# Kernel tuning notes

Measured on AMD Instinct MI355X. Metric: run time of the kernel, lower is better.

## Reference

```python
import jax, jax.numpy as jnp
import numpy as np

# Model constants (match init_kwargs)
DIM = 256
H = 8
HD = DIM // H          # 32
WIN = 5                # spatial window_size
QS = 4                 # quant_size
CQS = 2 * QS           # color_quant_size = 8
CWIN = 2               # color_windowsize
W = 64                 # voxels per window (equal-size windows for the reference)
L_XYZ = WIN * QS       # 20 -> table length 40
L_RGB = CWIN * CQS     # 16 -> table length 32


def setup_inputs() -> dict:
    key = jax.random.key(0)
    ks = jax.random.split(key, 12)
    N = 8192
    feats = jax.random.normal(ks[0], (N, DIM), dtype=jnp.float32)
    xyz = jax.random.uniform(ks[1], (N, 3), dtype=jnp.float32) * WIN    # [0, window_size)
    rgb = jax.random.uniform(ks[2], (N, 3), dtype=jnp.float32) * CWIN   # [0, color_windowsize)
    n_coords = jnp.concatenate([xyz, rgb], axis=1)
    std = 0.02
    xyz_shape = (3, 2 * L_XYZ, H, HD)
    rgb_shape = (3, 2 * L_RGB, H, HD)
    return {
        "feats": feats,
        "n_coords": n_coords,
        "qkv_w": jax.random.normal(ks[3], (3 * DIM, DIM), dtype=jnp.float32) * std,
        "qkv_b": jnp.zeros((3 * DIM,), dtype=jnp.float32),
        "q_xyz_t": jax.random.normal(ks[4], xyz_shape, dtype=jnp.float32) * std,
        "k_xyz_t": jax.random.normal(ks[5], xyz_shape, dtype=jnp.float32) * std,
        "v_xyz_t": jax.random.normal(ks[6], xyz_shape, dtype=jnp.float32) * std,
        "q_rgb_t": jax.random.normal(ks[7], rgb_shape, dtype=jnp.float32) * std,
        "k_rgb_t": jax.random.normal(ks[8], rgb_shape, dtype=jnp.float32) * std,
        "v_rgb_t": jax.random.normal(ks[9], rgb_shape, dtype=jnp.float32) * std,
        "proj_w": jax.random.normal(ks[10], (DIM, DIM), dtype=jnp.float32) * std,
        "proj_b": jnp.zeros((DIM,), dtype=jnp.float32),
    }


def _attn_bias(q, k, idx, q_table, k_table):
    """Relative-signal bias added to QK logits.
    q,k: [nw, W, H, hd]; idx: [nw, W, W, 3] int; tables: [3, T, H, hd].
    bias[n,h,i,j] = sum_c q[n,i,h]. q_table[c, idx[n,i,j,c], h] + k[n,j,h]. k_table[c, idx, h]
    Returns (bias [nw,H,W,W], one_hot [nw,W,W,3,T]) so the one-hot is reused for the value bias.
    """
    T = q_table.shape[1]
    oh = jax.nn.one_hot(idx, T, dtype=q.dtype)                # [nw,W,W,3,T]
    dq = jnp.einsum('nihd,cthd->nicht', q, q_table)           # per-voxel dot vs all table rows
    dk = jnp.einsum('njhd,cthd->njcht', k, k_table)
    bias_q = jnp.einsum('nicht,nijct->nhij', dq, oh)
    bias_k = jnp.einsum('njcht,nijct->nhij', dk, oh)
    return bias_q + bias_k, oh


def _value_bias(attn, oh, v_table):
    """out[n,i,h,:] += sum_j attn[n,h,i,j] * sum_c v_table[c, idx[n,i,j,c], h, :]"""
    at = jnp.einsum('nhij,nijct->nhict', attn, oh)            # scatter attn mass onto table rows
    return jnp.einsum('nhict,cthd->nihd', at, v_table)


def reference(feats, n_coords, qkv_w, qkv_b, q_xyz_t, k_xyz_t, v_xyz_t,
              q_rgb_t, k_rgb_t, v_rgb_t, proj_w, proj_b):
    N = feats.shape[0]
    nw = N // W
    scale = HD ** (-0.5)

    # QKV projection, split into per-window heads
    qkv = (feats @ qkv_w.T + qkv_b).reshape(nw, W, 3, H, HD)
    q = qkv[:, :, 0] * scale
    k = qkv[:, :, 1]
    v = qkv[:, :, 2]

    # Quantized relative-signal indices (coordinate deltas, offset to [0, 2L))
    scaled = jnp.concatenate(
        [n_coords[:, 0:3] * QS, n_coords[:, 3:6] * CQS], axis=1)   # [N, 6]
    cw = scaled.reshape(nw, W, 6)
    delta = jnp.floor(cw[:, :, None, :] - cw[:, None, :, :]).astype(jnp.int32)
    offs = jnp.array([L_XYZ] * 3 + [L_RGB] * 3, dtype=jnp.int32)
    hi = jnp.array([2 * L_XYZ - 1] * 3 + [2 * L_RGB - 1] * 3, dtype=jnp.int32)
    idx = jnp.clip(delta + offs, 0, hi)                        # [nw, W, W, 6]
    idx_xyz, idx_rgb = idx[..., :3], idx[..., 3:]

    bias_x, oh_x = _attn_bias(q, k, idx_xyz, q_xyz_t, k_xyz_t)
    bias_r, oh_r = _attn_bias(q, k, idx_rgb, q_rgb_t, k_rgb_t)

    logits = jnp.einsum('nihd,njhd->nhij', q, k) + bias_x + bias_r
    attn = jax.nn.softmax(logits, axis=-1)

    out = (jnp.einsum('nhij,njhd->nihd', attn, v)
           + _value_bias(attn, oh_x, v_xyz_t)
           + _value_bias(attn, oh_r, v_rgb_t))
    out = out.reshape(N, DIM)
    return out @ proj_w.T + proj_b
```

## Files before the change

### kernel.cpp

```cpp
#include <hip/hip_runtime.h>


typedef __attribute__((ext_vector_type(8))) short short8;
typedef __attribute__((ext_vector_type(4))) float f32x4;

__device__ __forceinline__ unsigned short f2bf(float f) {
    union { float f; unsigned int u; } v; v.f = f;
    unsigned int r = v.u + 0x7FFFu + ((v.u >> 16) & 1u);
    return (unsigned short)(r >> 16);
}

#define LFENCE() asm volatile("s_waitcnt lgkmcnt(0)" ::: "memory")

__global__ __launch_bounds__(256) void k_qkv(
    const float* __restrict__ A, const float* __restrict__ B,
    const float* __restrict__ bias,
    ushort* __restrict__ qb, ushort* __restrict__ kb, ushort* __restrict__ vb)
{
    __shared__ __align__(16) ushort a_s[128 * 72];
    __shared__ __align__(16) ushort b_s[64 * 72];
    const int tid = threadIdx.x;
    const int m0 = blockIdx.y * 128;
    const int n0 = blockIdx.x * 64;
    const int w = tid >> 6, wm = w >> 1, wn = w & 1;
    const int l4 = tid & 15, quad = (tid >> 4) & 3;
    f32x4 acc[4][2];
#pragma unroll
    for (int mt = 0; mt < 4; ++mt)
#pragma unroll
        for (int nt = 0; nt < 2; ++nt) acc[mt][nt] = (f32x4){0.f, 0.f, 0.f, 0.f};

    for (int k0 = 0; k0 < 256; k0 += 64) {
#pragma unroll
        for (int l = 0; l < 4; ++l) {
            int e = tid + l * 256;
            int row = e >> 3, kq = e & 7;
            const float* ap = A + (size_t)(m0 + row) * 256 + k0 + kq * 8;
            float4 v0 = *(const float4*)ap, v1 = *(const float4*)(ap + 4);
            union { ushort u[8]; uint4 v; } pk;
            pk.u[0] = f2bf(v0.x); pk.u[1] = f2bf(v0.y); pk.u[2] = f2bf(v0.z); pk.u[3] = f2bf(v0.w);
            pk.u[4] = f2bf(v1.x); pk.u[5] = f2bf(v1.y); pk.u[6] = f2bf(v1.z); pk.u[7] = f2bf(v1.w);
            *(uint4*)&a_s[row * 72 + kq * 8] = pk.v;
        }
#pragma unroll
        for (int l = 0; l < 2; ++l) {
            int e = tid + l * 256;
            int row = e >> 3, kq = e & 7;
            const float* bp = B + (size_t)(n0 + row) * 256 + k0 + kq * 8;
            float4 v0 = *(const float4*)bp, v1 = *(const float4*)(bp + 4);
            union { ushort u[8]; uint4 v; } pk;
            pk.u[0] = f2bf(v0.x); pk.u[1] = f2bf(v0.y); pk.u[2] = f2bf(v0.z); pk.u[3] = f2bf(v0.w);
            pk.u[4] = f2bf(v1.x); pk.u[5] = f2bf(v1.y); pk.u[6] = f2bf(v1.z); pk.u[7] = f2bf(v1.w);
            *(uint4*)&b_s[row * 72 + kq * 8] = pk.v;
        }
        __syncthreads();
#pragma unroll
        for (int kh = 0; kh < 2; ++kh) {
            short8 bf0 = *(const short8*)&b_s[(wn * 32 + l4) * 72 + kh * 32 + quad * 8];
            short8 bf1 = *(const short8*)&b_s[(wn * 32 + 16 + l4) * 72 + kh * 32 + quad * 8];
#pragma unroll
            for (int mt = 0; mt < 4; ++mt) {
                short8 af = *(const short8*)&a_s[(wm * 64 + mt * 16 + l4) * 72 + kh * 32 + quad * 8];
                acc[mt][0] = __builtin_amdgcn_mfma_f32_16x16x32_bf16(af, bf0, acc[mt][0], 0, 0, 0);
                acc[mt][1] = __builtin_amdgcn_mfma_f32_16x16x32_bf16(af, bf1, acc[mt][1], 0, 0, 0);
            }
        }
        __syncthreads();
    }
#pragma unroll
    for (int nt = 0; nt < 2; ++nt) {
        int c = n0 + wn * 32 + nt * 16 + l4;
        float bv = bias[c];
        int s = c >> 8, rem = c & 255, h = rem >> 5, d = rem & 31;
        ushort* dst = (s == 0) ? qb : ((s == 1) ? kb : vb);
        float mul = (s == 0) ? 0.17677669529663687f : 1.0f;
#pragma unroll
        for (int mt = 0; mt < 4; ++mt) {
            int mbase = m0 + wm * 64 + mt * 16 + quad * 4;
#pragma unroll
            for (int reg = 0; reg < 4; ++reg) {
                int m = mbase + reg;
                int nw = m >> 6, ii = m & 63;
                dst[((size_t)((nw * 8 + h) * 64 + ii)) * 32 + d] = f2bf((acc[mt][nt][reg] + bv) * mul);
            }
        }
    }
}

#define DBS 44
#define FXS 16777216.0f
#define FXI (1.0f / 16777216.0f)

__global__ __launch_bounds__(256, 2) void k_bias(
    const ushort* __restrict__ qb, const ushort* __restrict__ kb,
    const float* __restrict__ nco,
    const float* __restrict__ kxt, const float* __restrict__ krt,
    float* __restrict__ lgt)
{
    __shared__ __align__(16) float dbuf[64 * DBS];
    __shared__ __align__(16) ushort q_s[64 * 40];
    __shared__ __align__(16) ushort k_s[64 * 40];
    __shared__ __align__(16) ushort tbl[128 * 40];
    __shared__ __align__(16) float cwf[64 * 6];

    const int tid = threadIdx.x;
    const int n = blockIdx.x >> 3;
    const int h = blockIdx.x & 7;
    const int w = tid >> 6;
    const int l4 = tid & 15;
    const int quad = (tid >> 4) & 3;

    const size_t base = (size_t)((n * 8 + h) * 64) * 32;

    {
        int row = tid >> 2, part = tid & 3;
        *(uint4*)&q_s[row * 40 + part * 8] = *(const uint4*)(qb + base + tid * 8);
        *(uint4*)&k_s[row * 40 + part * 8] = *(const uint4*)(kb + base + tid * 8);
    }
    if (tid < 64) {
        const float* cp = nco + (size_t)(n * 64 + tid) * 6;
        cwf[tid * 6 + 0] = cp[0] * 4.f; cwf[tid * 6 + 1] = cp[1] * 4.f;
        cwf[tid * 6 + 2] = cp[2] * 4.f; cwf[tid * 6 + 3] = cp[3] * 8.f;
        cwf[tid * 6 + 4] = cp[4] * 8.f; cwf[tid * 6 + 5] = cp[5] * 8.f;
    }

    auto stageTbl = [&](const float* tbg, int R, int Rpad) {
        for (int e = tid; e < R * 4; e += 256) {
            int r = e >> 2, part = e & 3;
            const float* src = tbg + (size_t)r * 256 + part * 8;
            float4 f0 = *(const float4*)src, f1 = *(const float4*)(src + 4);
            union { ushort u[8]; uint4 v; } pk;
            pk.u[0] = f2bf(f0.x); pk.u[1] = f2bf(f0.y); pk.u[2] = f2bf(f0.z); pk.u[3] = f2bf(f0.w);
            pk.u[4] = f2bf(f1.x); pk.u[5] = f2bf(f1.y); pk.u[6] = f2bf(f1.z); pk.u[7] = f2bf(f1.w);
            *(uint4*)&tbl[r * 40 + part * 8] = pk.v;
        }
        for (int e = tid; e < (Rpad - R) * 40; e += 256) tbl[R * 40 + e] = 0;
    };

    float lg[4][4];
    int ibase[4];
#pragma unroll
    for (int r = 0; r < 4; ++r) ibase[r] = (w * 16 + quad * 4 + r) * DBS;

    auto tgemmC = [&](const ushort* a_s, int c, int T) {
        short8 af = *(const short8*)&a_s[(w * 16 + l4) * 40 + quad * 8];
        const int NT = (T == 40) ? 3 : 2;
        for (int tt = 0; tt < NT; ++tt) {
            short8 bf = *(const short8*)&tbl[(c * T + tt * 16 + l4) * 40 + quad * 8];
            f32x4 a = {0.f, 0.f, 0.f, 0.f};
            a = __builtin_amdgcn_mfma_f32_16x16x32_bf16(af, bf, a, 0, 0, 0);
            int col = tt * 16 + l4;
            int rb = w * 16 + quad * 4;
            if (col < T) {
                dbuf[(rb + 0) * DBS + col] = a[0];
                dbuf[(rb + 1) * DBS + col] = a[1];
                dbuf[(rb + 2) * DBS + col] = a[2];
                dbuf[(rb + 3) * DBS + col] = a[3];
            }
        }
    };

    stageTbl(kxt + h * 32, 120, 128);
    __syncthreads();

    unsigned idxp[24];
    {
        float co[4][6], cl[4][6];
#pragma unroll
        for (int r = 0; r < 4; ++r) {
            int j = w * 16 + quad * 4 + r;
#pragma unroll
            for (int c6 = 0; c6 < 6; ++c6) co[r][c6] = cwf[j * 6 + c6];
        }
#pragma unroll
        for (int tt = 0; tt < 4; ++tt) {
            int i = tt * 16 + l4;
#pragma unroll
            for (int c6 = 0; c6 < 6; ++c6) cl[tt][c6] = cwf[i * 6 + c6];
        }
#pragma unroll
        for (int c6 = 0; c6 < 6; ++c6) {
            const int off = (c6 < 3) ? 20 : 16, hi = (c6 < 3) ? 39 : 31;
#pragma unroll
            for (int tt = 0; tt < 4; ++tt) {
                unsigned p = 0;
#pragma unroll
                for (int r = 0; r < 4; ++r) {
                    int x = min(max((int)floorf(cl[tt][c6] - co[r][c6]) + off, 0), hi);
                    p |= (unsigned)x << (8 * r);
                }
                idxp[c6 * 4 + tt] = p;
            }
        }
    }

    auto gatherT = [&](int cc) {
#pragma unroll
        for (int tt = 0; tt < 4; ++tt) {
            unsigned p = idxp[cc * 4 + tt];
#pragma unroll
            for (int r = 0; r < 4; ++r) {
                int x = (p >> (8 * r)) & 255;
                lg[tt][r] += dbuf[ibase[r] + x];
            }
        }
    };

    {
        short8 ak = *(const short8*)&k_s[(w * 16 + l4) * 40 + quad * 8];
#pragma unroll
        for (int tt = 0; tt < 4; ++tt) {
            short8 bq = *(const short8*)&q_s[(tt * 16 + l4) * 40 + quad * 8];
            f32x4 r = {0.f, 0.f, 0.f, 0.f};
            r = __builtin_amdgcn_mfma_f32_16x16x32_bf16(ak, bq, r, 0, 0, 0);
            lg[tt][0] = r[0]; lg[tt][1] = r[1]; lg[tt][2] = r[2]; lg[tt][3] = r[3];
        }
    }

    tgemmC(k_s, 0, 40); LFENCE();
    gatherT(0); LFENCE();
    tgemmC(k_s, 1, 40); LFENCE();
    gatherT(1); LFENCE();
    tgemmC(k_s, 2, 40); LFENCE();
    gatherT(2);
    __syncthreads();
    stageTbl(krt + h * 32, 96, 96);
    __syncthreads();
    tgemmC(k_s, 0, 32); LFENCE();
    gatherT(3); LFENCE();
    tgemmC(k_s, 1, 32); LFENCE();
    gatherT(4); LFENCE();
    tgemmC(k_s, 2, 32); LFENCE();
    gatherT(5);

    {
        float* lp = lgt + (size_t)(n * 8 + h) * 4096;
#pragma unroll
        for (int tt = 0; tt < 4; ++tt)
#pragma unroll
            for (int reg = 0; reg < 4; ++reg)
                lp[(w * 16 + quad * 4 + reg) * 64 + tt * 16 + l4] = lg[tt][reg];
    }
}

__global__ __launch_bounds__(256, 2) void k_av(
    const ushort* __restrict__ qb, const ushort* __restrict__ vb,
    const float* __restrict__ nco,
    const float* __restrict__ qxt, const float* __restrict__ vxt,
    const float* __restrict__ qrt, const float* __restrict__ vrt,
    const float* __restrict__ lgt,
    ushort* __restrict__ aout)
{
    __shared__ __align__(16) float dbuf[64 * DBS];
    __shared__ __align__(16) ushort U[11264];
    __shared__ __align__(16) float cwf[64 * 6];
    ushort* q_s  = U;
    ushort* tbl  = U + 2560;
    ushort* attn_s = U;
    ushort* v_t    = U + 4608;
    ushort* vtbl   = U + 6912;

    const int tid = threadIdx.x;
    const int n = blockIdx.x >> 3;
    const int h = blockIdx.x & 7;
    const int w = tid >> 6;
    const int lane = tid & 63;
    const int l4 = tid & 15;
    const int quad = (tid >> 4) & 3;

    const size_t base = (size_t)((n * 8 + h) * 64) * 32;

    {
        int row = tid >> 2, part = tid & 3;
        *(uint4*)&q_s[row * 40 + part * 8] = *(const uint4*)(qb + base + tid * 8);
    }
    if (tid < 64) {
        const float* cp = nco + (size_t)(n * 64 + tid) * 6;
        cwf[tid * 6 + 0] = cp[0] * 4.f; cwf[tid * 6 + 1] = cp[1] * 4.f;
        cwf[tid * 6 + 2] = cp[2] * 4.f; cwf[tid * 6 + 3] = cp[3] * 8.f;
        cwf[tid * 6 + 4] = cp[4] * 8.f; cwf[tid * 6 + 5] = cp[5] * 8.f;
    }

    auto stageTbl = [&](const float* tbg, int R, int Rpad) {
        for (int e = tid; e < R * 4; e += 256) {
            int r = e >> 2, part = e & 3;
            const float* src = tbg + (size_t)r * 256 + part * 8;
            float4 f0 = *(const float4*)src, f1 = *(const float4*)(src + 4);
            union { ushort u[8]; uint4 v; } pk;
            pk.u[0] = f2bf(f0.x); pk.u[1] = f2bf(f0.y); pk.u[2] = f2bf(f0.z); pk.u[3] = f2bf(f0.w);
            pk.u[4] = f2bf(f1.x); pk.u[5] = f2bf(f1.y); pk.u[6] = f2bf(f1.z); pk.u[7] = f2bf(f1.w);
            *(uint4*)&tbl[r * 40 + part * 8] = pk.v;
        }
        for (int e = tid; e < (Rpad - R) * 40; e += 256) tbl[R * 40 + e] = 0;
    };
    auto stageVtbl = [&](const float* tbg, int R) {
        for (int e = tid; e < R * 4; e += 256) {
            int r = e >> 2, part = e & 3;
            const float* src = tbg + (size_t)r * 256 + part * 8;
            float4 f0 = *(const float4*)src, f1 = *(const float4*)(src + 4);
            int d0 = part * 8;
            vtbl[(d0 + 0) * 136 + r] = f2bf(f0.x);
            vtbl[(d0 + 1) * 136 + r] = f2bf(f0.y);
            vtbl[(d0 + 2) * 136 + r] = f2bf(f0.z);
            vtbl[(d0 + 3) * 136 + r] = f2bf(f0.w);
            vtbl[(d0 + 4) * 136 + r] = f2bf(f1.x);
            vtbl[(d0 + 5) * 136 + r] = f2bf(f1.y);
            vtbl[(d0 + 6) * 136 + r] = f2bf(f1.z);
            vtbl[(d0 + 7) * 136 + r] = f2bf(f1.w);
        }
    };
    auto stageVt = [&]() {
        int j = tid >> 2, d0 = (tid & 3) * 8;
        uint4 pk = *(const uint4*)(vb + base + tid * 8);
        const ushort* u = (const ushort*)&pk;
#pragma unroll
        for (int ii = 0; ii < 8; ++ii) v_t[(d0 + ii) * 72 + j] = u[ii];
    };

    float lg[4][4];
    {
        const float* lp = lgt + (size_t)(n * 8 + h) * 4096;
        int i0 = w * 16 + quad * 4;
#pragma unroll
        for (int tt = 0; tt < 4; ++tt) {
            f32x4 v = *(const f32x4*)(lp + (size_t)(tt * 16 + l4) * 64 + i0);
            lg[tt][0] = v[0]; lg[tt][1] = v[1]; lg[tt][2] = v[2]; lg[tt][3] = v[3];
        }
    }

    int ibase[4];
#pragma unroll
    for (int r = 0; r < 4; ++r) ibase[r] = (w * 16 + quad * 4 + r) * DBS;

    auto tgemmC = [&](const ushort* a_s, int c, int T) {
        short8 af = *(const short8*)&a_s[(w * 16 + l4) * 40 + quad * 8];
        const int NT = (T == 40) ? 3 : 2;
        for (int tt = 0; tt < NT; ++tt) {
            short8 bf = *(const short8*)&tbl[(c * T + tt * 16 + l4) * 40 + quad * 8];
            f32x4 a = {0.f, 0.f, 0.f, 0.f};
            a = __builtin_amdgcn_mfma_f32_16x16x32_bf16(af, bf, a, 0, 0, 0);
            int col = tt * 16 + l4;
            int rb = w * 16 + quad * 4;
            if (col < T) {
                dbuf[(rb + 0) * DBS + col] = a[0];
                dbuf[(rb + 1) * DBS + col] = a[1];
                dbuf[(rb + 2) * DBS + col] = a[2];
                dbuf[(rb + 3) * DBS + col] = a[3];
            }
        }
    };
    auto zeroOwn = [&]() {
        float4 z = {0.f, 0.f, 0.f, 0.f};
        float4* rb = (float4*)&dbuf[w * 16 * DBS];
        for (int v = lane; v < 176; v += 64) rb[v] = z;
    };

    stageTbl(qxt + h * 32, 120, 128);
    __syncthreads();

    unsigned idxp[24];
    {
        float co[4][6], cl[4][6];
#pragma unroll
        for (int r = 0; r < 4; ++r) {
            int i = w * 16 + quad * 4 + r;
#pragma unroll
            for (int c6 = 0; c6 < 6; ++c6) co[r][c6] = cwf[i * 6 + c6];
        }
#pragma unroll
        for (int tt = 0; tt < 4; ++tt) {
            int j = tt * 16 + l4;
#pragma unroll
            for (int c6 = 0; c6 < 6; ++c6) cl[tt][c6] = cwf[j * 6 + c6];
        }
#pragma unroll
        for (int c6 = 0; c6 < 6; ++c6) {
            const int off = (c6 < 3) ? 20 : 16, hi = (c6 < 3) ? 39 : 31;
#pragma unroll
            for (int tt = 0; tt < 4; ++tt) {
                unsigned p = 0;
#pragma unroll
                for (int r = 0; r < 4; ++r) {
                    int x = min(max((int)floorf(co[r][c6] - cl[tt][c6]) + off, 0), hi);
                    p |= (unsigned)x << (8 * r);
                }
                idxp[c6 * 4 + tt] = p;
            }
        }
    }

    auto gatherC = [&](int cc) {
#pragma unroll
        for (int tt = 0; tt < 4; ++tt) {
            unsigned p = idxp[cc * 4 + tt];
#pragma unroll
            for (int r = 0; r < 4; ++r) {
                int x = (p >> (8 * r)) & 255;
                lg[tt][r] += dbuf[ibase[r] + x];
            }
        }
    };
    auto scatterC = [&](int cc) {
        unsigned* bb = (unsigned*)dbuf;
#pragma unroll
        for (int tt = 0; tt < 4; ++tt) {
            unsigned p = idxp[cc * 4 + tt];
#pragma unroll
            for (int r = 0; r < 4; ++r) {
                int x = (p >> (8 * r)) & 255;
                unsigned q = (unsigned)(lg[tt][r] * FXS + 0.5f);
                atomicAdd(&bb[ibase[r] + x], q);
            }
        }
    };

    tgemmC(q_s, 0, 40); LFENCE();
    gatherC(0); LFENCE();
    tgemmC(q_s, 1, 40); LFENCE();
    gatherC(1); LFENCE();
    tgemmC(q_s, 2, 40);
    __syncthreads();
    gatherC(2);
    stageTbl(qrt + h * 32, 96, 96);
    __syncthreads();
    tgemmC(q_s, 0, 32); LFENCE();
    gatherC(3); LFENCE();
    tgemmC(q_s, 1, 32); LFENCE();
    gatherC(4); LFENCE();
    tgemmC(q_s, 2, 32);
    __syncthreads();
    gatherC(5);
    stageVtbl(vxt + h * 32, 120);
    stageVt();
    __syncthreads();

#pragma unroll
    for (int reg = 0; reg < 4; ++reg) {
        float m = fmaxf(fmaxf(lg[0][reg], lg[1][reg]), fmaxf(lg[2][reg], lg[3][reg]));
        m = fmaxf(m, __shfl_xor(m, 1));
        m = fmaxf(m, __shfl_xor(m, 2));
        m = fmaxf(m, __shfl_xor(m, 4));
        m = fmaxf(m, __shfl_xor(m, 8));
        float s = 0.f;
#pragma unroll
        for (int tt = 0; tt < 4; ++tt) { lg[tt][reg] = __expf(lg[tt][reg] - m); s += lg[tt][reg]; }
        s += __shfl_xor(s, 1); s += __shfl_xor(s, 2);
        s += __shfl_xor(s, 4); s += __shfl_xor(s, 8);
        float inv = 1.f / s;
#pragma unroll
        for (int tt = 0; tt < 4; ++tt) lg[tt][reg] *= inv;
    }
#pragma unroll
    for (int tt = 0; tt < 4; ++tt)
#pragma unroll
        for (int reg = 0; reg < 4; ++reg)
            attn_s[(w * 16 + quad * 4 + reg) * 72 + tt * 16 + l4] = f2bf(lg[tt][reg]);
    zeroOwn();
    __syncthreads();

    f32x4 acc0 = {0.f, 0.f, 0.f, 0.f}, acc1 = {0.f, 0.f, 0.f, 0.f};
#pragma unroll
    for (int s = 0; s < 2; ++s) {
        short8 af = *(const short8*)&attn_s[(w * 16 + l4) * 72 + s * 32 + quad * 8];
        short8 b0 = *(const short8*)&v_t[l4 * 72 + s * 32 + quad * 8];
        short8 b1 = *(const short8*)&v_t[(16 + l4) * 72 + s * 32 + quad * 8];
        acc0 = __builtin_amdgcn_mfma_f32_16x16x32_bf16(af, b0, acc0, 0, 0, 0);
        acc1 = __builtin_amdgcn_mfma_f32_16x16x32_bf16(af, b1, acc1, 0, 0, 0);
    }

    auto atgemmC = [&](int c, int T, int S) {
#pragma unroll
        for (int s = 0; s < S; ++s) {
            int koff = s * 32 + quad * 8;
            short8 af = {0, 0, 0, 0, 0, 0, 0, 0};
            int kr = 0;
            if (koff < T) {
                const unsigned* ap = (const unsigned*)&dbuf[(w * 16 + l4) * DBS + koff];
                uint4 u0 = *(const uint4*)ap;
                uint4 u1 = *(const uint4*)(ap + 4);
                af[0] = (short)f2bf((float)u0.x * FXI); af[1] = (short)f2bf((float)u0.y * FXI);
                af[2] = (short)f2bf((float)u0.z * FXI); af[3] = (short)f2bf((float)u0.w * FXI);
                af[4] = (short)f2bf((float)u1.x * FXI); af[5] = (short)f2bf((float)u1.y * FXI);
                af[6] = (short)f2bf((float)u1.z * FXI); af[7] = (short)f2bf((float)u1.w * FXI);
                kr = c * T + koff;
            }
            short8 b0 = *(const short8*)&vtbl[l4 * 136 + kr];
            short8 b1 = *(const short8*)&vtbl[(16 + l4) * 136 + kr];
            acc0 = __builtin_amdgcn_mfma_f32_16x16x32_bf16(af, b0, acc0, 0, 0, 0);
            acc1 = __builtin_amdgcn_mfma_f32_16x16x32_bf16(af, b1, acc1, 0, 0, 0);
        }
    };

    scatterC(0); LFENCE();
    atgemmC(0, 40, 2); LFENCE();
    zeroOwn(); LFENCE();
    scatterC(1); LFENCE();
    atgemmC(1, 40, 2); LFENCE();
    zeroOwn(); LFENCE();
    scatterC(2); LFENCE();
    atgemmC(2, 40, 2);
    __syncthreads();
    zeroOwn();
    stageVtbl(vrt + h * 32, 96);
    __syncthreads();

    scatterC(3); LFENCE();
    atgemmC(0, 32, 1); LFENCE();
    zeroOwn(); LFENCE();
    scatterC(4); LFENCE();
    atgemmC(1, 32, 1); LFENCE();
    zeroOwn(); LFENCE();
    scatterC(5); LFENCE();
    atgemmC(2, 32, 1);

    {
        ushort* op = aout + (size_t)(n * 64 + w * 16 + quad * 4) * 256 + h * 32;
#pragma unroll
        for (int reg = 0; reg < 4; ++reg) {
            op[reg * 256 + l4] = f2bf(acc0[reg]);
            op[reg * 256 + 16 + l4] = f2bf(acc1[reg]);
        }
    }
}

__global__ __launch_bounds__(256) void k_proj(
    const ushort* __restrict__ A, const float* __restrict__ B,
    const float* __restrict__ bias, float* __restrict__ out)
{
    __shared__ __align__(16) ushort a_s[128 * 72];
    __shared__ __align__(16) ushort b_s[64 * 72];
    const int tid = threadIdx.x;
    const int m0 = blockIdx.y * 128;
    const int n0 = blockIdx.x * 64;
    const int w = tid >> 6, wm = w >> 1, wn = w & 1;
    const int l4 = tid & 15, quad = (tid >> 4) & 3;
    f32x4 acc[4][2];
#pragma unroll
    for (int mt = 0; mt < 4; ++mt)
#pragma unroll
        for (int nt = 0; nt < 2; ++nt) acc[mt][nt] = (f32x4){0.f, 0.f, 0.f, 0.f};

    for (int k0 = 0; k0 < 256; k0 += 64) {
#pragma unroll
        for (int l = 0; l < 4; ++l) {
            int e = tid + l * 256;
            int row = e >> 3, kq = e & 7;
            *(uint4*)&a_s[row * 72 + kq * 8] =
                *(const uint4*)(A + (size_t)(m0 + row) * 256 + k0 + kq * 8);
        }
#pragma unroll
        for (int l = 0; l < 2; ++l) {
            int e = tid + l * 256;
            int row = e >> 3, kq = e & 7;
            const float* bp = B + (size_t)(n0 + row) * 256 + k0 + kq * 8;
            float4 v0 = *(const float4*)bp, v1 = *(const float4*)(bp + 4);
            union { ushort u[8]; uint4 v; } pk;
            pk.u[0] = f2bf(v0.x); pk.u[1] = f2bf(v0.y); pk.u[2] = f2bf(v0.z); pk.u[3] = f2bf(v0.w);
            pk.u[4] = f2bf(v1.x); pk.u[5] = f2bf(v1.y); pk.u[6] = f2bf(v1.z); pk.u[7] = f2bf(v1.w);
            *(uint4*)&b_s[row * 72 + kq * 8] = pk.v;
        }
        __syncthreads();
#pragma unroll
        for (int kh = 0; kh < 2; ++kh) {
            short8 bf0 = *(const short8*)&b_s[(wn * 32 + l4) * 72 + kh * 32 + quad * 8];
            short8 bf1 = *(const short8*)&b_s[(wn * 32 + 16 + l4) * 72 + kh * 32 + quad * 8];
#pragma unroll
            for (int mt = 0; mt < 4; ++mt) {
                short8 af = *(const short8*)&a_s[(wm * 64 + mt * 16 + l4) * 72 + kh * 32 + quad * 8];
                acc[mt][0] = __builtin_amdgcn_mfma_f32_16x16x32_bf16(af, bf0, acc[mt][0], 0, 0, 0);
                acc[mt][1] = __builtin_amdgcn_mfma_f32_16x16x32_bf16(af, bf1, acc[mt][1], 0, 0, 0);
            }
        }
        __syncthreads();
    }
#pragma unroll
    for (int nt = 0; nt < 2; ++nt) {
        int c = n0 + wn * 32 + nt * 16 + l4;
        float bv = bias[c];
#pragma unroll
        for (int mt = 0; mt < 4; ++mt) {
            int mbase = m0 + wm * 64 + mt * 16 + quad * 4;
#pragma unroll
            for (int reg = 0; reg < 4; ++reg)
                out[(size_t)(mbase + reg) * 256 + c] = acc[mt][nt][reg] + bv;
        }
    }
}

extern "C" void kernel_launch(void* const* d_in, const int* in_sizes, int n_in,
                              void* d_out, int out_size, void* d_ws, size_t ws_size,
                              hipStream_t stream)
{
    const float* feats = (const float*)d_in[0];
    const float* nco   = (const float*)d_in[1];
    const float* qkvw  = (const float*)d_in[2];
    const float* qkvb  = (const float*)d_in[3];
    const float* qxt   = (const float*)d_in[4];
    const float* kxt   = (const float*)d_in[5];
    const float* vxt   = (const float*)d_in[6];
    const float* qrt   = (const float*)d_in[7];
    const float* krt   = (const float*)d_in[8];
    const float* vrt   = (const float*)d_in[9];
    const float* pw    = (const float*)d_in[10];
    const float* pb    = (const float*)d_in[11];
    float* out = (float*)d_out;

    ushort* qb  = (ushort*)d_ws;
    ushort* kb  = qb + (size_t)2097152;
    ushort* vb  = kb + (size_t)2097152;
    ushort* aob = vb + (size_t)2097152;
    float*  lgt = (float*)(aob + (size_t)2097152);

    k_qkv<<<dim3(12, 64), 256, 0, stream>>>(feats, qkvw, qkvb, qb, kb, vb);
    k_bias<<<dim3(1024), 256, 0, stream>>>(qb, kb, nco, kxt, krt, lgt);
    k_av<<<dim3(1024), 256, 0, stream>>>(qb, vb, nco, qxt, vxt, qrt, vrt, lgt, aob);
    k_proj<<<dim3(4, 64), 256, 0, stream>>>(aob, pw, pb, out);
}
```

Baseline: 153.7 us.

## Pre-cast GEMM operands to bf16 in a separate kernel and halve M tiles

Adds a k_cast kernel that converts feats, qkv_w and proj_w to bf16 once. The QKV and projection GEMMs then load bf16 directly instead of re-converting fp32 weights in every block. Both GEMMs also drop from 128-row to 64-row M tiles, doubling the grid for better CU occupancy. The cost is an extra launch, an extra round trip of feats through global memory, and less A/B reuse per block.

```diff
diff --git a/kernel.cpp b/kernel.cpp
--- a/kernel.cpp
+++ b/kernel.cpp
@@ -12,46 +12,51 @@
 
 #define LFENCE() asm volatile("s_waitcnt lgkmcnt(0)" ::: "memory")
 
+__global__ __launch_bounds__(256) void k_cast(
+    const float* __restrict__ feats, const float* __restrict__ qkvw,
+    const float* __restrict__ pw,
+    ushort* __restrict__ fb, ushort* __restrict__ qwb, ushort* __restrict__ pwb)
+{
+    int t = blockIdx.x * 256 + threadIdx.x;
+    const float* src; ushort* dst; int off;
+    if (t < 262144)            { src = feats; dst = fb;  off = t; }
+    else if (t < 286720)       { src = qkvw;  dst = qwb; off = t - 262144; }
+    else                       { src = pw;    dst = pwb; off = t - 286720; }
+    const float* s = src + (size_t)off * 8;
+    float4 v0 = *(const float4*)s, v1 = *(const float4*)(s + 4);
+    union { ushort u[8]; uint4 v; } pk;
+    pk.u[0] = f2bf(v0.x); pk.u[1] = f2bf(v0.y); pk.u[2] = f2bf(v0.z); pk.u[3] = f2bf(v0.w);
+    pk.u[4] = f2bf(v1.x); pk.u[5] = f2bf(v1.y); pk.u[6] = f2bf(v1.z); pk.u[7] = f2bf(v1.w);
+    *(uint4*)(dst + (size_t)off * 8) = pk.v;
+}
+
 __global__ __launch_bounds__(256) void k_qkv(
-    const float* __restrict__ A, const float* __restrict__ B,
+    const ushort* __restrict__ A, const ushort* __restrict__ B,
     const float* __restrict__ bias,
     ushort* __restrict__ qb, ushort* __restrict__ kb, ushort* __restrict__ vb)
 {
-    __shared__ __align__(16) ushort a_s[128 * 72];
+    __shared__ __align__(16) ushort a_s[64 * 72];
     __shared__ __align__(16) ushort b_s[64 * 72];
     const int tid = threadIdx.x;
-    const int m0 = blockIdx.y * 128;
+    const int m0 = blockIdx.y * 64;
     const int n0 = blockIdx.x * 64;
     const int w = tid >> 6, wm = w >> 1, wn = w & 1;
     const int l4 = tid & 15, quad = (tid >> 4) & 3;
-    f32x4 acc[4][2];
-#pragma unroll
-    for (int mt = 0; mt < 4; ++mt)
+    f32x4 acc[2][2];
+#pragma unroll
+    for (int mt = 0; mt < 2; ++mt)
 #pragma unroll
         for (int nt = 0; nt < 2; ++nt) acc[mt][nt] = (f32x4){0.f, 0.f, 0.f, 0.f};
 
     for (int k0 = 0; k0 < 256; k0 += 64) {
-#pragma unroll
-        for (int l = 0; l < 4; ++l) {
-            int e = tid + l * 256;
-            int row = e >> 3, kq = e & 7;
-            const float* ap = A + (size_t)(m0 + row) * 256 + k0 + kq * 8;
-            float4 v0 = *(const float4*)ap, v1 = *(const float4*)(ap + 4);
-            union { ushort u[8]; uint4 v; } pk;
-            pk.u[0] = f2bf(v0.x); pk.u[1] = f2bf(v0.y); pk.u[2] = f2bf(v0.z); pk.u[3] = f2bf(v0.w);
-            pk.u[4] = f2bf(v1.x); pk.u[5] = f2bf(v1.y); pk.u[6] = f2bf(v1.z); pk.u[7] = f2bf(v1.w);
-            *(uint4*)&a_s[row * 72 + kq * 8] = pk.v;
-        }
 #pragma unroll
         for (int l = 0; l < 2; ++l) {
             int e = tid + l * 256;
             int row = e >> 3, kq = e & 7;
-            const float* bp = B + (size_t)(n0 + row) * 256 + k0 + kq * 8;
-            float4 v0 = *(const float4*)bp, v1 = *(const float4*)(bp + 4);
-            union { ushort u[8]; uint4 v; } pk;
-            pk.u[0] = f2bf(v0.x); pk.u[1] = f2bf(v0.y); pk.u[2] = f2bf(v0.z); pk.u[3] = f2bf(v0.w);
-            pk.u[4] = f2bf(v1.x); pk.u[5] = f2bf(v1.y); pk.u[6] = f2bf(v1.z); pk.u[7] = f2bf(v1.w);
-            *(uint4*)&b_s[row * 72 + kq * 8] = pk.v;
+            *(uint4*)&a_s[row * 72 + kq * 8] =
+                *(const uint4*)(A + (size_t)(m0 + row) * 256 + k0 + kq * 8);
+            *(uint4*)&b_s[row * 72 + kq * 8] =
+                *(const uint4*)(B + (size_t)(n0 + row) * 256 + k0 + kq * 8);
         }
         __syncthreads();
 #pragma unroll
@@ -59,8 +64,8 @@
             short8 bf0 = *(const short8*)&b_s[(wn * 32 + l4) * 72 + kh * 32 + quad * 8];
             short8 bf1 = *(const short8*)&b_s[(wn * 32 + 16 + l4) * 72 + kh * 32 + quad * 8];
 #pragma unroll
-            for (int mt = 0; mt < 4; ++mt) {
-                short8 af = *(const short8*)&a_s[(wm * 64 + mt * 16 + l4) * 72 + kh * 32 + quad * 8];
+            for (int mt = 0; mt < 2; ++mt) {
+                short8 af = *(const short8*)&a_s[(wm * 32 + mt * 16 + l4) * 72 + kh * 32 + quad * 8];
                 acc[mt][0] = __builtin_amdgcn_mfma_f32_16x16x32_bf16(af, bf0, acc[mt][0], 0, 0, 0);
                 acc[mt][1] = __builtin_amdgcn_mfma_f32_16x16x32_bf16(af, bf1, acc[mt][1], 0, 0, 0);
             }
@@ -75,8 +80,8 @@
         ushort* dst = (s == 0) ? qb : ((s == 1) ? kb : vb);
         float mul = (s == 0) ? 0.17677669529663687f : 1.0f;
 #pragma unroll
-        for (int mt = 0; mt < 4; ++mt) {
-            int mbase = m0 + wm * 64 + mt * 16 + quad * 4;
+        for (int mt = 0; mt < 2; ++mt) {
+            int mbase = m0 + wm * 32 + mt * 16 + quad * 4;
 #pragma unroll
             for (int reg = 0; reg < 4; ++reg) {
                 int m = mbase + reg;
@@ -524,40 +529,31 @@
 }
 
 __global__ __launch_bounds__(256) void k_proj(
-    const ushort* __restrict__ A, const float* __restrict__ B,
+    const ushort* __restrict__ A, const ushort* __restrict__ B,
     const float* __restrict__ bias, float* __restrict__ out)
 {
-    __shared__ __align__(16) ushort a_s[128 * 72];
+    __shared__ __align__(16) ushort a_s[64 * 72];
     __shared__ __align__(16) ushort b_s[64 * 72];
     const int tid = threadIdx.x;
-    const int m0 = blockIdx.y * 128;
+    const int m0 = blockIdx.y * 64;
     const int n0 = blockIdx.x * 64;
     const int w = tid >> 6, wm = w >> 1, wn = w & 1;
     const int l4 = tid & 15, quad = (tid >> 4) & 3;
-    f32x4 acc[4][2];
-#pragma unroll
-    for (int mt = 0; mt < 4; ++mt)
+    f32x4 acc[2][2];
+#pragma unroll
+    for (int mt = 0; mt < 2; ++mt)
 #pragma unroll
         for (int nt = 0; nt < 2; ++nt) acc[mt][nt] = (f32x4){0.f, 0.f, 0.f, 0.f};
 
     for (int k0 = 0; k0 < 256; k0 += 64) {
 #pragma unroll
-        for (int l = 0; l < 4; ++l) {
+        for (int l = 0; l < 2; ++l) {
             int e = tid + l * 256;
             int row = e >> 3, kq = e & 7;
             *(uint4*)&a_s[row * 72 + kq * 8] =
                 *(const uint4*)(A + (size_t)(m0 + row) * 256 + k0 + kq * 8);
-        }
-#pragma unroll
-        for (int l = 0; l < 2; ++l) {
-            int e = tid + l * 256;
-            int row = e >> 3, kq = e & 7;
-            const float* bp = B + (size_t)(n0 + row) * 256 + k0 + kq * 8;
-            float4 v0 = *(const float4*)bp, v1 = *(const float4*)(bp + 4);
-            union { ushort u[8]; uint4 v; } pk;
-            pk.u[0] = f2bf(v0.x); pk.u[1] = f2bf(v0.y); pk.u[2] = f2bf(v0.z); pk.u[3] = f2bf(v0.w);
-            pk.u[4] = f2bf(v1.x); pk.u[5] = f2bf(v1.y); pk.u[6] = f2bf(v1.z); pk.u[7] = f2bf(v1.w);
-            *(uint4*)&b_s[row * 72 + kq * 8] = pk.v;
+            *(uint4*)&b_s[row * 72 + kq * 8] =
+                *(const uint4*)(B + (size_t)(n0 + row) * 256 + k0 + kq * 8);
         }
         __syncthreads();
 #pragma unroll
@@ -565,8 +561,8 @@
             short8 bf0 = *(const short8*)&b_s[(wn * 32 + l4) * 72 + kh * 32 + quad * 8];
             short8 bf1 = *(const short8*)&b_s[(wn * 32 + 16 + l4) * 72 + kh * 32 + quad * 8];
 #pragma unroll
-            for (int mt = 0; mt < 4; ++mt) {
-                short8 af = *(const short8*)&a_s[(wm * 64 + mt * 16 + l4) * 72 + kh * 32 + quad * 8];
+            for (int mt = 0; mt < 2; ++mt) {
+                short8 af = *(const short8*)&a_s[(wm * 32 + mt * 16 + l4) * 72 + kh * 32 + quad * 8];
                 acc[mt][0] = __builtin_amdgcn_mfma_f32_16x16x32_bf16(af, bf0, acc[mt][0], 0, 0, 0);
                 acc[mt][1] = __builtin_amdgcn_mfma_f32_16x16x32_bf16(af, bf1, acc[mt][1], 0, 0, 0);
             }
@@ -578,8 +574,8 @@
         int c = n0 + wn * 32 + nt * 16 + l4;
         float bv = bias[c];
 #pragma unroll
-        for (int mt = 0; mt < 4; ++mt) {
-            int mbase = m0 + wm * 64 + mt * 16 + quad * 4;
+        for (int mt = 0; mt < 2; ++mt) {
+            int mbase = m0 + wm * 32 + mt * 16 + quad * 4;
 #pragma unroll
             for (int reg = 0; reg < 4; ++reg)
                 out[(size_t)(mbase + reg) * 256 + c] = acc[mt][nt][reg] + bv;
@@ -610,9 +606,13 @@
     ushort* vb  = kb + (size_t)2097152;
     ushort* aob = vb + (size_t)2097152;
     float*  lgt = (float*)(aob + (size_t)2097152);
-
-    k_qkv<<<dim3(12, 64), 256, 0, stream>>>(feats, qkvw, qkvb, qb, kb, vb);
+    ushort* fb  = (ushort*)(lgt + (size_t)4194304);
+    ushort* qwb = fb + (size_t)2097152;
+    ushort* pwb = qwb + (size_t)196608;
+
+    k_cast<<<dim3(1152), 256, 0, stream>>>(feats, qkvw, pw, fb, qwb, pwb);
+    k_qkv<<<dim3(12, 128), 256, 0, stream>>>(fb, qwb, qkvb, qb, kb, vb);
     k_bias<<<dim3(1024), 256, 0, stream>>>(qb, kb, nco, kxt, krt, lgt);
     k_av<<<dim3(1024), 256, 0, stream>>>(qb, vb, nco, qxt, vxt, qrt, vrt, lgt, aob);
-    k_proj<<<dim3(4, 64), 256, 0, stream>>>(aob, pw, pb, out);
+    k_proj<<<dim3(4, 128), 256, 0, stream>>>(aob, pwb, pb, out);
 }
```

Result: faster. 149.1 us (-3.0%).
